# Kernel optimization log

Measured on AMD Instinct MI355X. Metric: run time of the kernel, lower is better.

Reference implementation:

```python
import jax, jax.numpy as jnp
import numpy as np
import math


def setup_inputs() -> dict:
    key = jax.random.key(0)
    ks = jax.random.split(key, 5)
    B, C, E = 4, 2048, 1024
    max_len = 2048
    s = 1.0 / math.sqrt(E)
    return {
        "x": jax.random.normal(ks[0], (B, C, E), dtype=jnp.float32),
        "W_q": jax.random.normal(ks[1], (E, E), dtype=jnp.float32) * s,
        "W_k": jax.random.normal(ks[2], (E, E), dtype=jnp.float32) * s,
        "W_v": jax.random.normal(ks[3], (E, E), dtype=jnp.float32) * s,
        "rel_bias": jax.random.normal(ks[4], (2 * max_len - 1, 1), dtype=jnp.float32),
        "max_len": max_len,
    }


def reference(x, W_q, W_k, W_v, rel_bias, max_len):
    B, C, E = x.shape
    # nn.Linear(bias=False): y = x @ W.T
    Q = jnp.einsum("bce,fe->bcf", x, W_q)
    K = jnp.einsum("bce,fe->bcf", x, W_k)
    V = jnp.einsum("bce,fe->bcf", x, W_v)
    scores = jnp.einsum("bqe,bke->bqk", Q, K) / math.sqrt(E)
    pos = jnp.arange(C)
    rel_dist = jnp.clip(pos[None, :] - pos[:, None] + (max_len - 1), 0, 2 * max_len - 2)
    bias = rel_bias[rel_dist, 0]  # [C, C]
    scores = scores + bias[None, :, :]
    weights = jax.nn.softmax(scores, axis=-1)
    out = jnp.einsum("bqk,bke->bqe", weights, V)
    return out, weights
```

## Files before the change

### kernel.cpp

```cpp
#include <hip/hip_runtime.h>
#include <hip/hip_bf16.h>
#include <math.h>

typedef __attribute__((ext_vector_type(8))) short short8;
typedef __attribute__((ext_vector_type(4))) short short4v;
typedef __attribute__((ext_vector_type(4))) float f32x4;

static __device__ __forceinline__ short f2bf(float f) {
  union { float f; unsigned u; } x;
  x.f = f;
  unsigned r = x.u + 0x7fffu + ((x.u >> 16) & 1u);
  return (short)(r >> 16);
}

#define GLD16(g, l)                                                   \
  __builtin_amdgcn_global_load_lds(                                   \
      (const __attribute__((address_space(1))) void*)(g),             \
      (__attribute__((address_space(3))) void*)(l), 16, 0, 0)
#define BAR() asm volatile("s_barrier" ::: "memory")
#define VMCNT6() asm volatile("s_waitcnt vmcnt(6)" ::: "memory")
#define VMCNT0() asm volatile("s_waitcnt vmcnt(0)" ::: "memory")

__global__ __launch_bounds__(256) void cvt_all(
    const float* __restrict__ x, const float* __restrict__ wq,
    const float* __restrict__ wk, const float* __restrict__ wv,
    short* __restrict__ xb, short* __restrict__ wqb,
    short* __restrict__ wkb, short* __restrict__ wvb, int n0, int n1) {
  int i = blockIdx.x * 256 + threadIdx.x;
  const float* src; short* dst; int off;
  if (i < n0) { src = x; dst = xb; off = i; }
  else if (i < n0 + n1) { src = wq; dst = wqb; off = i - n0; }
  else if (i < n0 + 2 * n1) { src = wk; dst = wkb; off = i - n0 - n1; }
  else if (i < n0 + 3 * n1) { src = wv; dst = wvb; off = i - n0 - 2 * n1; }
  else return;
  const float4* p = (const float4*)src + (size_t)off * 2;
  float4 a = p[0], b = p[1];
  short8 o;
  o[0] = f2bf(a.x); o[1] = f2bf(a.y); o[2] = f2bf(a.z); o[3] = f2bf(a.w);
  o[4] = f2bf(b.x); o[5] = f2bf(b.y); o[6] = f2bf(b.z); o[7] = f2bf(b.w);
  *((short8*)dst + off) = o;
}

template <int MODE>
__global__ __launch_bounds__(512) void gemm3b(
    const short* __restrict__ A, const short* __restrict__ Bt,
    void* __restrict__ C0, void* __restrict__ C1, void* __restrict__ C2,
    const float* __restrict__ rel_bias,
    int N, int K, long aZ, long bZ, long cZ, int Cdim, float scale, int ml) {
  __shared__ short sA[3][256 * 64];
  __shared__ short sB[3][128 * 64];
  const int tid = threadIdx.x, lane = tid & 63, wid = tid >> 6;

  const int gx = gridDim.x, gy = gridDim.y;
  const int nwg = gx * gy * (int)gridDim.z;
  const int f = ((int)blockIdx.z * gy + (int)blockIdx.y) * gx + (int)blockIdx.x;
  const int qq = nwg >> 3, rr = nwg & 7;
  const int xcd = f & 7, pos = f >> 3;
  const int lg = (xcd < rr ? xcd * (qq + 1) : rr * (qq + 1) + (xcd - rr) * qq) + pos;
  const int z = lg / (gx * gy);
  const int rem = lg - z * (gx * gy);
  const int bx = rem / gy, by = rem - bx * gy;

  const short* Az = A + (size_t)z * aZ;
  const short* Bz = Bt + (size_t)z * bZ;
  const int brow = bx * 256, bcol = by * 128;
  const int wr = wid >> 2, wc = wid & 3;
  const int lrow = lane & 15, kg = lane >> 4;
  const int l8 = lane >> 3, lm8 = lane & 7;
  const int scol = (lm8 ^ l8) * 8;

  const short* aS[2][2];
  int aD[2][2];
#pragma unroll
  for (int h = 0; h < 2; ++h)
#pragma unroll
    for (int j = 0; j < 2; ++j) {
      int c = wid * 2 + j;
      int rb = c * 8 + (c >= 8 ? 64 : 0) + h * 64;
      aS[h][j] = Az + (size_t)(brow + rb + l8) * K + scol;
      aD[h][j] = rb * 64;
    }
  const short* bS[2];
  int bD[2];
#pragma unroll
  for (int h = 0; h < 2; ++h) {
    int rb = wid * 8 + h * 64;
    bS[h] = Bz + (size_t)(bcol + rb + l8) * K + scol;
    bD[h] = rb * 64;
  }

  const int sks0 = ((0 + kg) ^ (lrow & 7)) * 8;
  const int sks1 = ((4 + kg) ^ (lrow & 7)) * 8;
  const int aR = (wr * 128 + lrow) * 64;
  const int bR = (wc * 32 + lrow) * 64;

  short8 a[4][2], b[2][2];
  f32x4 acc[8][2] = {};

  short *pa0 = &sA[0][0], *pa1 = &sA[1][0], *pa2 = &sA[2][0];
  short *pb0 = &sB[0][0], *pb1 = &sB[1][0], *pb2 = &sB[2][0];

#define STG_A(PA, H, T)                                          \
  do {                                                           \
    GLD16(aS[H][0] + (size_t)(T) * 64, (PA) + aD[H][0]);         \
    GLD16(aS[H][1] + (size_t)(T) * 64, (PA) + aD[H][1]);         \
  } while (0)
#define STG_B(PB, H, T) GLD16(bS[H] + (size_t)(T) * 64, (PB) + bD[H])
#define RD_A(PA, MH)                                                          \
  do {                                                                        \
    _Pragma("unroll") for (int mq = 0; mq < 4; ++mq) {                        \
      a[mq][0] = *(const short8*)&(PA)[aR + (MH)*4096 + mq * 1024 + sks0];    \
      a[mq][1] = *(const short8*)&(PA)[aR + (MH)*4096 + mq * 1024 + sks1];    \
    }                                                                         \
  } while (0)
#define RD_B(PB)                                                   \
  do {                                                             \
    _Pragma("unroll") for (int nq = 0; nq < 2; ++nq) {             \
      b[nq][0] = *(const short8*)&(PB)[bR + nq * 1024 + sks0];     \
      b[nq][1] = *(const short8*)&(PB)[bR + nq * 1024 + sks1];     \
    }                                                              \
  } while (0)
#define MFMA16(MH)                                                            \
  do {                                                                        \
    __builtin_amdgcn_s_setprio(1);                                            \
    _Pragma("unroll") for (int mq = 0; mq < 4; ++mq)                          \
        _Pragma("unroll") for (int nq = 0; nq < 2; ++nq) {                    \
      acc[(MH)*4 + mq][nq] = __builtin_amdgcn_mfma_f32_16x16x32_bf16(         \
          a[mq][0], b[nq][0], acc[(MH)*4 + mq][nq], 0, 0, 0);                 \
      acc[(MH)*4 + mq][nq] = __builtin_amdgcn_mfma_f32_16x16x32_bf16(         \
          a[mq][1], b[nq][1], acc[(MH)*4 + mq][nq], 0, 0, 0);                 \
    }                                                                         \
    __builtin_amdgcn_s_setprio(0);                                            \
  } while (0)

  STG_A(pa0, 0, 0); STG_B(pb0, 0, 0); STG_A(pa0, 1, 0); STG_B(pb0, 1, 0);
  STG_A(pa1, 0, 1); STG_B(pb1, 0, 1); STG_A(pa1, 1, 1); STG_B(pb1, 1, 1);
  VMCNT6();
  BAR();

  const int NT = K >> 6;
  for (int t = 0; t < NT - 2; ++t) {
    RD_A(pa0, 0); RD_B(pb0);
    STG_A(pa2, 0, t + 2); STG_B(pb2, 0, t + 2);
    BAR();
    MFMA16(0);
    BAR();
    RD_A(pa0, 1);
    STG_A(pa2, 1, t + 2); STG_B(pb2, 1, t + 2);
    VMCNT6();
    BAR();
    MFMA16(1);
    BAR();
    short* q;
    q = pa0; pa0 = pa1; pa1 = pa2; pa2 = q;
    q = pb0; pb0 = pb1; pb1 = pb2; pb2 = q;
  }
  RD_A(pa0, 0); RD_B(pb0);
  BAR(); MFMA16(0); BAR();
  RD_A(pa0, 1);
  VMCNT0();
  BAR(); MFMA16(1); BAR();
  RD_A(pa1, 0); RD_B(pb1);
  BAR(); MFMA16(0); BAR();
  RD_A(pa1, 1);
  BAR(); MFMA16(1);

#pragma unroll
  for (int m = 0; m < 8; ++m) {
#pragma unroll
    for (int n = 0; n < 2; ++n) {
#pragma unroll
      for (int r = 0; r < 4; ++r) {
        float v = acc[m][n][r];
        int gr = brow + wr * 128 + m * 16 + kg * 4 + r;
        int gc = bcol + wc * 32 + n * 16 + lrow;
        if constexpr (MODE == 2) {
          int idx = gc - gr + (ml - 1);
          idx = min(max(idx, 0), 2 * ml - 2);
          ((float*)C0 + (size_t)z * cZ)[(size_t)gr * N + gc] =
              v * scale + rel_bias[idx];
        } else if constexpr (MODE == 3) {
          ((float*)C0 + (size_t)z * cZ)[(size_t)gr * N + gc] = v;
        } else {
          int s = gc >> 10, cc = gc & 1023;
          short* dst = (s == 0) ? (short*)C0 : (s == 1) ? (short*)C1 : (short*)C2;
          dst[(size_t)gr * 1024 + cc] = f2bf(v);
        }
      }
    }
  }
#undef STG_A
#undef STG_B
#undef RD_A
#undef RD_B
#undef MFMA16
}

__global__ __launch_bounds__(256) void transpose_v(const short* __restrict__ vin,
                                                   short* __restrict__ vout,
                                                   int Cd, int E) {
  __shared__ short t[64][72];
  const int c0 = blockIdx.x * 64, e0 = blockIdx.y * 64, b = blockIdx.z;
  const int tid = threadIdx.x;
  const int cr = tid >> 2;
  const int ec = (tid & 3) * 16;
  const short* src = vin + ((size_t)b * Cd + c0 + cr) * E + e0 + ec;
  short8 v0 = *(const short8*)src;
  short8 v1 = *(const short8*)(src + 8);
#pragma unroll
  for (int j = 0; j < 8; ++j) t[ec + j][cr] = v0[j];
#pragma unroll
  for (int j = 0; j < 8; ++j) t[ec + 8 + j][cr] = v1[j];
  __syncthreads();
  const int er = tid >> 2;
  const int cc = (tid & 3) * 16;
  short* dst = vout + ((size_t)b * E + e0 + er) * Cd + c0 + cc;
  *(short8*)dst = *(const short8*)&t[er][cc];
  *(short8*)(dst + 8) = *(const short8*)&t[er][cc + 8];
}

__global__ __launch_bounds__(256) void softmax_rows(float* __restrict__ w,
                                                    short* __restrict__ wb, int Cd) {
  const size_t row = blockIdx.x;
  float4* p = (float4*)(w + row * (size_t)Cd);
  const int tid = threadIdx.x;
  float4 v0 = p[tid];
  float4 v1 = p[tid + 256];
  float mx = fmaxf(fmaxf(fmaxf(v0.x, v0.y), fmaxf(v0.z, v0.w)),
                   fmaxf(fmaxf(v1.x, v1.y), fmaxf(v1.z, v1.w)));
#pragma unroll
  for (int o = 32; o; o >>= 1) mx = fmaxf(mx, __shfl_xor(mx, o));
  __shared__ float red[8];
  const int wv = tid >> 6;
  if ((tid & 63) == 0) red[wv] = mx;
  __syncthreads();
  mx = fmaxf(fmaxf(red[0], red[1]), fmaxf(red[2], red[3]));
  v0.x = __expf(v0.x - mx); v0.y = __expf(v0.y - mx);
  v0.z = __expf(v0.z - mx); v0.w = __expf(v0.w - mx);
  v1.x = __expf(v1.x - mx); v1.y = __expf(v1.y - mx);
  v1.z = __expf(v1.z - mx); v1.w = __expf(v1.w - mx);
  float s = v0.x + v0.y + v0.z + v0.w + v1.x + v1.y + v1.z + v1.w;
#pragma unroll
  for (int o = 32; o; o >>= 1) s += __shfl_xor(s, o);
  if ((tid & 63) == 0) red[4 + wv] = s;
  __syncthreads();
  s = red[4] + red[5] + red[6] + red[7];
  float inv = 1.0f / s;
  v0.x *= inv; v0.y *= inv; v0.z *= inv; v0.w *= inv;
  v1.x *= inv; v1.y *= inv; v1.z *= inv; v1.w *= inv;
  p[tid] = v0;
  p[tid + 256] = v1;
  short4v b0, b1;
  b0[0] = f2bf(v0.x); b0[1] = f2bf(v0.y); b0[2] = f2bf(v0.z); b0[3] = f2bf(v0.w);
  b1[0] = f2bf(v1.x); b1[1] = f2bf(v1.y); b1[2] = f2bf(v1.z); b1[3] = f2bf(v1.w);
  short* wrow = wb + row * (size_t)Cd;
  *(short4v*)&wrow[tid * 4] = b0;
  *(short4v*)&wrow[1024 + tid * 4] = b1;
}

extern "C" void kernel_launch(void* const* d_in, const int* in_sizes, int n_in,
                              void* d_out, int out_size, void* d_ws, size_t ws_size,
                              hipStream_t stream) {
  const float* x = (const float*)d_in[0];
  const float* Wq = (const float*)d_in[1];
  const float* Wk = (const float*)d_in[2];
  const float* Wv = (const float*)d_in[3];
  const float* rb = (const float*)d_in[4];

  const int E = 1024;
  const int Mt = in_sizes[0] / E;
  const int Cd = out_size / Mt - E;
  const int B = Mt / Cd;
  const int ml = (in_sizes[4] + 1) / 2;
  const float scale = 1.0f / sqrtf((float)E);

  short* xb = (short*)d_ws;
  short* wqb = xb + (size_t)Mt * E;
  short* wkb = wqb + (size_t)E * E;
  short* wvb = wkb + (size_t)E * E;
  short* Qb = wvb + (size_t)E * E;
  short* Kb = Qb + (size_t)Mt * E;
  short* Vrow = Kb + (size_t)Mt * E;
  short* Vt = xb;
  short* wbf = Qb;

  float* outp = (float*)d_out;
  float* wts = outp + (size_t)Mt * E;

  const int n0 = (Mt * E) / 8, n1 = (E * E) / 8;
  cvt_all<<<(n0 + 3 * n1 + 255) / 256, 256, 0, stream>>>(
      x, Wq, Wk, Wv, xb, wqb, wkb, wvb, n0, n1);

  dim3 blk(512);
  gemm3b<4><<<dim3(Mt / 256, 3 * E / 128, 1), blk, 0, stream>>>(
      xb, wqb, Qb, Kb, Vrow, nullptr, 3 * E, E, 0, 0, 0, Cd, 0.f, ml);
  gemm3b<2><<<dim3(Cd / 256, Cd / 128, B), blk, 0, stream>>>(
      Qb, Kb, wts, nullptr, nullptr, rb, Cd, E, (long)Cd * E, (long)Cd * E,
      (long)Cd * Cd, Cd, scale, ml);
  softmax_rows<<<Mt, 256, 0, stream>>>(wts, wbf, Cd);
  transpose_v<<<dim3(Cd / 64, E / 64, B), 256, 0, stream>>>(Vrow, Vt, Cd, E);
  gemm3b<3><<<dim3(Cd / 256, E / 128, B), blk, 0, stream>>>(
      wbf, Vt, outp, nullptr, nullptr, nullptr, E, Cd, (long)Cd * Cd,
      (long)E * Cd, (long)Cd * E, Cd, 0.f, ml);
}
```

Baseline: 199.8 us.

## Replace 256x128 GEMM tiles with 128x128 K32 tiles for higher occupancy

Rewrites the shared GEMM kernel to use 256-thread blocks computing 128x128 output tiles with a K-step of 32, a new XOR swizzle, and a single barrier per iteration in a triple-buffered pipeline. Launch bounds request three workgroups per CU so more blocks can overlap memory and MFMA work. In exchange, each block gets less operand reuse per loaded byte and the grids double in block count, with more frequent barriers per unit of K.

```diff
diff --git a/kernel.cpp b/kernel.cpp
--- a/kernel.cpp
+++ b/kernel.cpp
@@ -18,7 +18,7 @@
       (const __attribute__((address_space(1))) void*)(g),             \
       (__attribute__((address_space(3))) void*)(l), 16, 0, 0)
 #define BAR() asm volatile("s_barrier" ::: "memory")
-#define VMCNT6() asm volatile("s_waitcnt vmcnt(6)" ::: "memory")
+#define VMCNT4() asm volatile("s_waitcnt vmcnt(4)" ::: "memory")
 #define VMCNT0() asm volatile("s_waitcnt vmcnt(0)" ::: "memory")
 
 __global__ __launch_bounds__(256) void cvt_all(
@@ -42,13 +42,13 @@
 }
 
 template <int MODE>
-__global__ __launch_bounds__(512) void gemm3b(
+__global__ __launch_bounds__(256, 3) void gemm_oc(
     const short* __restrict__ A, const short* __restrict__ Bt,
     void* __restrict__ C0, void* __restrict__ C1, void* __restrict__ C2,
     const float* __restrict__ rel_bias,
     int N, int K, long aZ, long bZ, long cZ, int Cdim, float scale, int ml) {
-  __shared__ short sA[3][256 * 64];
-  __shared__ short sB[3][128 * 64];
+  __shared__ short sA[3][128 * 32];
+  __shared__ short sB[3][128 * 32];
   const int tid = threadIdx.x, lane = tid & 63, wid = tid >> 6;
 
   const int gx = gridDim.x, gy = gridDim.y;
@@ -63,117 +63,89 @@
 
   const short* Az = A + (size_t)z * aZ;
   const short* Bz = Bt + (size_t)z * bZ;
-  const int brow = bx * 256, bcol = by * 128;
-  const int wr = wid >> 2, wc = wid & 3;
+  const int brow = bx * 128, bcol = by * 128;
+  const int wr = wid >> 1, wc = wid & 1;
   const int lrow = lane & 15, kg = lane >> 4;
-  const int l8 = lane >> 3, lm8 = lane & 7;
-  const int scol = (lm8 ^ l8) * 8;
-
-  const short* aS[2][2];
-  int aD[2][2];
-#pragma unroll
-  for (int h = 0; h < 2; ++h)
-#pragma unroll
-    for (int j = 0; j < 2; ++j) {
-      int c = wid * 2 + j;
-      int rb = c * 8 + (c >= 8 ? 64 : 0) + h * 64;
-      aS[h][j] = Az + (size_t)(brow + rb + l8) * K + scol;
-      aD[h][j] = rb * 64;
-    }
-  const short* bS[2];
-  int bD[2];
-#pragma unroll
-  for (int h = 0; h < 2; ++h) {
-    int rb = wid * 8 + h * 64;
-    bS[h] = Bz + (size_t)(bcol + rb + l8) * K + scol;
-    bD[h] = rb * 64;
-  }
-
-  const int sks0 = ((0 + kg) ^ (lrow & 7)) * 8;
-  const int sks1 = ((4 + kg) ^ (lrow & 7)) * 8;
-  const int aR = (wr * 128 + lrow) * 64;
-  const int bR = (wc * 32 + lrow) * 64;
-
-  short8 a[4][2], b[2][2];
-  f32x4 acc[8][2] = {};
+
+  const int t4 = tid >> 2;
+  const int logslot = (tid & 3) ^ ((tid >> 3) & 3);
+  const short* aSrc0 = Az + (size_t)(brow + t4) * K + logslot * 8;
+  const short* aSrc1 = Az + (size_t)(brow + 64 + t4) * K + logslot * 8;
+  const short* bSrc0 = Bz + (size_t)(bcol + t4) * K + logslot * 8;
+  const short* bSrc1 = Bz + (size_t)(bcol + 64 + t4) * K + logslot * 8;
+  const int d0 = wid * 512, d1 = 2048 + wid * 512;
+
+  const int kOff = (kg ^ ((lrow >> 1) & 3)) * 8;
+  const int aBase = (wr * 64 + lrow) * 32 + kOff;
+  const int bBase = (wc * 64 + lrow) * 32 + kOff;
+
+  short8 a[4], b[4];
+  f32x4 acc[4][4] = {};
 
   short *pa0 = &sA[0][0], *pa1 = &sA[1][0], *pa2 = &sA[2][0];
   short *pb0 = &sB[0][0], *pb1 = &sB[1][0], *pb2 = &sB[2][0];
 
-#define STG_A(PA, H, T)                                          \
-  do {                                                           \
-    GLD16(aS[H][0] + (size_t)(T) * 64, (PA) + aD[H][0]);         \
-    GLD16(aS[H][1] + (size_t)(T) * 64, (PA) + aD[H][1]);         \
-  } while (0)
-#define STG_B(PB, H, T) GLD16(bS[H] + (size_t)(T) * 64, (PB) + bD[H])
-#define RD_A(PA, MH)                                                          \
-  do {                                                                        \
-    _Pragma("unroll") for (int mq = 0; mq < 4; ++mq) {                        \
-      a[mq][0] = *(const short8*)&(PA)[aR + (MH)*4096 + mq * 1024 + sks0];    \
-      a[mq][1] = *(const short8*)&(PA)[aR + (MH)*4096 + mq * 1024 + sks1];    \
-    }                                                                         \
-  } while (0)
-#define RD_B(PB)                                                   \
-  do {                                                             \
-    _Pragma("unroll") for (int nq = 0; nq < 2; ++nq) {             \
-      b[nq][0] = *(const short8*)&(PB)[bR + nq * 1024 + sks0];     \
-      b[nq][1] = *(const short8*)&(PB)[bR + nq * 1024 + sks1];     \
-    }                                                              \
-  } while (0)
-#define MFMA16(MH)                                                            \
+#define STG(PA, PB, T)                                    \
+  do {                                                    \
+    GLD16(aSrc0 + (size_t)(T) * 32, (PA) + d0);           \
+    GLD16(aSrc1 + (size_t)(T) * 32, (PA) + d1);           \
+    GLD16(bSrc0 + (size_t)(T) * 32, (PB) + d0);           \
+    GLD16(bSrc1 + (size_t)(T) * 32, (PB) + d1);           \
+  } while (0)
+#define RD(PA, PB)                                                  \
+  do {                                                              \
+    _Pragma("unroll") for (int m = 0; m < 4; ++m)                   \
+        a[m] = *(const short8*)&(PA)[aBase + m * 512];              \
+    _Pragma("unroll") for (int n = 0; n < 4; ++n)                   \
+        b[n] = *(const short8*)&(PB)[bBase + n * 512];              \
+  } while (0)
+#define MFMA16()                                                              \
   do {                                                                        \
     __builtin_amdgcn_s_setprio(1);                                            \
-    _Pragma("unroll") for (int mq = 0; mq < 4; ++mq)                          \
-        _Pragma("unroll") for (int nq = 0; nq < 2; ++nq) {                    \
-      acc[(MH)*4 + mq][nq] = __builtin_amdgcn_mfma_f32_16x16x32_bf16(         \
-          a[mq][0], b[nq][0], acc[(MH)*4 + mq][nq], 0, 0, 0);                 \
-      acc[(MH)*4 + mq][nq] = __builtin_amdgcn_mfma_f32_16x16x32_bf16(         \
-          a[mq][1], b[nq][1], acc[(MH)*4 + mq][nq], 0, 0, 0);                 \
-    }                                                                         \
+    _Pragma("unroll") for (int m = 0; m < 4; ++m)                             \
+        _Pragma("unroll") for (int n = 0; n < 4; ++n)                         \
+            acc[m][n] = __builtin_amdgcn_mfma_f32_16x16x32_bf16(              \
+                a[m], b[n], acc[m][n], 0, 0, 0);                              \
     __builtin_amdgcn_s_setprio(0);                                            \
   } while (0)
-
-  STG_A(pa0, 0, 0); STG_B(pb0, 0, 0); STG_A(pa0, 1, 0); STG_B(pb0, 1, 0);
-  STG_A(pa1, 0, 1); STG_B(pb1, 0, 1); STG_A(pa1, 1, 1); STG_B(pb1, 1, 1);
-  VMCNT6();
+#define ROT()                                                    \
+  do {                                                           \
+    short* q;                                                    \
+    q = pa0; pa0 = pa1; pa1 = pa2; pa2 = q;                      \
+    q = pb0; pb0 = pb1; pb1 = pb2; pb2 = q;                      \
+  } while (0)
+
+  STG(pa0, pb0, 0);
+  STG(pa1, pb1, 1);
+
+  const int NT = K >> 5;
+  for (int t = 0; t < NT - 2; ++t) {
+    VMCNT4();
+    BAR();
+    RD(pa0, pb0);
+    STG(pa2, pb2, t + 2);
+    MFMA16();
+    ROT();
+  }
+  VMCNT4();
   BAR();
-
-  const int NT = K >> 6;
-  for (int t = 0; t < NT - 2; ++t) {
-    RD_A(pa0, 0); RD_B(pb0);
-    STG_A(pa2, 0, t + 2); STG_B(pb2, 0, t + 2);
-    BAR();
-    MFMA16(0);
-    BAR();
-    RD_A(pa0, 1);
-    STG_A(pa2, 1, t + 2); STG_B(pb2, 1, t + 2);
-    VMCNT6();
-    BAR();
-    MFMA16(1);
-    BAR();
-    short* q;
-    q = pa0; pa0 = pa1; pa1 = pa2; pa2 = q;
-    q = pb0; pb0 = pb1; pb1 = pb2; pb2 = q;
-  }
-  RD_A(pa0, 0); RD_B(pb0);
-  BAR(); MFMA16(0); BAR();
-  RD_A(pa0, 1);
+  RD(pa0, pb0);
+  MFMA16();
+  ROT();
   VMCNT0();
-  BAR(); MFMA16(1); BAR();
-  RD_A(pa1, 0); RD_B(pb1);
-  BAR(); MFMA16(0); BAR();
-  RD_A(pa1, 1);
-  BAR(); MFMA16(1);
-
-#pragma unroll
-  for (int m = 0; m < 8; ++m) {
-#pragma unroll
-    for (int n = 0; n < 2; ++n) {
+  BAR();
+  RD(pa0, pb0);
+  MFMA16();
+
+#pragma unroll
+  for (int m = 0; m < 4; ++m) {
+#pragma unroll
+    for (int n = 0; n < 4; ++n) {
 #pragma unroll
       for (int r = 0; r < 4; ++r) {
         float v = acc[m][n][r];
-        int gr = brow + wr * 128 + m * 16 + kg * 4 + r;
-        int gc = bcol + wc * 32 + n * 16 + lrow;
+        int gr = brow + wr * 64 + m * 16 + kg * 4 + r;
+        int gc = bcol + wc * 64 + n * 16 + lrow;
         if constexpr (MODE == 2) {
           int idx = gc - gr + (ml - 1);
           idx = min(max(idx, 0), 2 * ml - 2);
@@ -189,11 +161,10 @@
       }
     }
   }
-#undef STG_A
-#undef STG_B
-#undef RD_A
-#undef RD_B
+#undef STG
+#undef RD
 #undef MFMA16
+#undef ROT
 }
 
 __global__ __launch_bounds__(256) void transpose_v(const short* __restrict__ vin,
@@ -291,15 +262,15 @@
   cvt_all<<<(n0 + 3 * n1 + 255) / 256, 256, 0, stream>>>(
       x, Wq, Wk, Wv, xb, wqb, wkb, wvb, n0, n1);
 
-  dim3 blk(512);
-  gemm3b<4><<<dim3(Mt / 256, 3 * E / 128, 1), blk, 0, stream>>>(
+  dim3 blk(256);
+  gemm_oc<4><<<dim3(Mt / 128, 3 * E / 128, 1), blk, 0, stream>>>(
       xb, wqb, Qb, Kb, Vrow, nullptr, 3 * E, E, 0, 0, 0, Cd, 0.f, ml);
-  gemm3b<2><<<dim3(Cd / 256, Cd / 128, B), blk, 0, stream>>>(
+  gemm_oc<2><<<dim3(Cd / 128, Cd / 128, B), blk, 0, stream>>>(
       Qb, Kb, wts, nullptr, nullptr, rb, Cd, E, (long)Cd * E, (long)Cd * E,
       (long)Cd * Cd, Cd, scale, ml);
   softmax_rows<<<Mt, 256, 0, stream>>>(wts, wbf, Cd);
   transpose_v<<<dim3(Cd / 64, E / 64, B), 256, 0, stream>>>(Vrow, Vt, Cd, E);
-  gemm3b<3><<<dim3(Cd / 256, E / 128, B), blk, 0, stream>>>(
+  gemm_oc<3><<<dim3(Cd / 128, E / 128, B), blk, 0, stream>>>(
       wbf, Vt, outp, nullptr, nullptr, nullptr, E, Cd, (long)Cd * Cd,
       (long)E * Cd, (long)Cd * E, Cd, 0.f, ml);
 }
```

After: 198.3 us. Within noise of the previous version (-0.7%).
